# Kernel tuning notes

Measured on AMD Instinct MI355X. Metric: run time of the kernel, lower is better.

## Reference

```python
import jax, jax.numpy as jnp
import numpy as np

TAU = 0.1      # Gumbel-Sinkhorn temperature (module default)
N_ITER = 100   # Sinkhorn iterations (module default)
B, N = 16, 256


def setup_inputs() -> dict:
    key = jax.random.key(0)
    alpha = jax.random.normal(key, (B, N, N), dtype=jnp.float32)
    return {"alpha": alpha}


def _log_sinkhorn(log_alpha, n_iter):
    # Successive row / column normalization in log space.
    # Note: the torch original early-exits once the column sums are within
    # eps=1e-6 of 1; once converged, further iterations are (numerically)
    # identity, so a fixed n_iter loop computes the same result. We use a
    # fixed-length lax.scan, which runs the whole loop on-device with no
    # per-step host sync.
    def step(la, _):
        la = la - jax.nn.logsumexp(la, axis=-1, keepdims=True)  # row normalize
        la = la - jax.nn.logsumexp(la, axis=-2, keepdims=True)  # col normalize
        return la, None

    log_alpha, _ = jax.lax.scan(step, log_alpha, None, length=n_iter)
    return jnp.exp(log_alpha)


def reference(alpha):
    # Training path of GumbelSinkhornPermutation.forward:
    # scale by temperature, then Sinkhorn-normalize to a near doubly-stochastic
    # matrix. (wandb logging side effects omitted.)
    return _log_sinkhorn(alpha / TAU, N_ITER)
```

## Files before the change

kernel.cpp:

```cpp
#include <hip/hip_runtime.h>

#define N_ITER 100

typedef float f32x4 __attribute__((ext_vector_type(4)));
typedef unsigned u32x4 __attribute__((ext_vector_type(4)));

__device__ __forceinline__ unsigned bf16pack(float a, float b) {
  unsigned ua = __float_as_uint(a), ub = __float_as_uint(b);
  ua = (ua + 0x7FFFu + ((ua >> 16) & 1u)) >> 16;
  ub = (ub + 0x7FFFu + ((ub >> 16) & 1u)) >> 16;
  return ua | (ub << 16);
}
__device__ __forceinline__ float bflo(unsigned u) { return __uint_as_float(u << 16); }
__device__ __forceinline__ float bfhi(unsigned u) { return __uint_as_float(u & 0xFFFF0000u); }

__device__ __forceinline__ void pin_agpr(u32x4& x) {
  asm("" : "=a"(x) : "0"(x));
}

__device__ __forceinline__ void mfma_first_nop(f32x4& acc, const u32x4& a, const u32x4& b) {
  asm("s_nop 2\n\tv_mfma_f32_16x16x32_bf16 %0, %1, %2, 0"
      : "=&v"(acc) : "a"(a), "v"(b));
}
__device__ __forceinline__ void mfma_first(f32x4& acc, const u32x4& a, const u32x4& b) {
  asm("v_mfma_f32_16x16x32_bf16 %0, %1, %2, 0"
      : "=&v"(acc) : "a"(a), "v"(b));
}
__device__ __forceinline__ void mfma_aa(f32x4& acc, const u32x4& a, const u32x4& b) {
  asm("v_mfma_f32_16x16x32_bf16 %0, %1, %2, %0"
      : "+v"(acc) : "a"(a), "v"(b));
}
__device__ __forceinline__ void mfma_fence4(f32x4& a0, f32x4& a1, f32x4& a2, f32x4& a3) {
  asm volatile("s_nop 7\n\ts_nop 7\n\ts_nop 7"
               : "+v"(a0), "+v"(a1), "+v"(a2), "+v"(a3));
}

__global__ __launch_bounds__(256)
__attribute__((amdgpu_waves_per_eu(1, 1)))
void sinkhorn_mfma4w(const float* __restrict__ alpha, float* __restrict__ out) {
  __shared__ alignas(16) unsigned short Cb16[256];
  __shared__ alignas(16) unsigned short Rb16[256];
  __shared__ alignas(16) float Cb32[256];
  __shared__ alignas(16) float Rb32[256];

  const int tid  = threadIdx.x;
  const int lane = tid & 63;
  const int w    = tid >> 6;
  const int m    = lane & 15;
  const int q    = lane >> 4;

  const size_t mbase = (size_t)blockIdx.x * (256 * 256);
  const float* A = alpha + mbase;
  float*       O = out + mbase;

  u32x4 arow[4][8];
  u32x4 acol[4][8];

#pragma unroll
  for (int s = 0; s < 4; ++s) {
    const float* rowp = A + (size_t)(64 * w + 16 * s + m) * 256 + 8 * q;
#pragma unroll
    for (int c = 0; c < 8; ++c) {
      float4 x0 = *(const float4*)(rowp + 32 * c);
      float4 x1 = *(const float4*)(rowp + 32 * c + 4);
      arow[s][c] = (u32x4){bf16pack(__expf(x0.x * 10.0f), __expf(x0.y * 10.0f)),
                           bf16pack(__expf(x0.z * 10.0f), __expf(x0.w * 10.0f)),
                           bf16pack(__expf(x1.x * 10.0f), __expf(x1.y * 10.0f)),
                           bf16pack(__expf(x1.z * 10.0f), __expf(x1.w * 10.0f))};
      pin_agpr(arow[s][c]);
    }
    const float* colp = A + (size_t)(8 * q) * 256 + 64 * w + 16 * s + m;
#pragma unroll
    for (int c = 0; c < 8; ++c) {
      const float* p = colp + (size_t)(32 * c) * 256;
      acol[s][c] =
          (u32x4){bf16pack(__expf(p[0] * 10.0f), __expf(p[256] * 10.0f)),
                  bf16pack(__expf(p[512] * 10.0f), __expf(p[768] * 10.0f)),
                  bf16pack(__expf(p[1024] * 10.0f), __expf(p[1280] * 10.0f)),
                  bf16pack(__expf(p[1536] * 10.0f), __expf(p[1792] * 10.0f))};
      pin_agpr(acol[s][c]);
    }
  }

  Cb16[tid] = 0x3F80;
  __syncthreads();

  for (int it = 0; it < N_ITER; ++it) {
    const bool last = (it == N_ITER - 1);

    {
      u32x4 B[8];
#pragma unroll
      for (int c = 0; c < 8; ++c) B[c] = *(const u32x4*)&Cb16[32 * c + 8 * q];
      f32x4 acc0, acc1, acc2, acc3;
      mfma_first_nop(acc0, arow[0][0], B[0]);
      mfma_first(acc1, arow[1][0], B[0]);
      mfma_first(acc2, arow[2][0], B[0]);
      mfma_first(acc3, arow[3][0], B[0]);
#pragma unroll
      for (int c = 1; c < 8; ++c) {
        mfma_aa(acc0, arow[0][c], B[c]);
        mfma_aa(acc1, arow[1][c], B[c]);
        mfma_aa(acc2, arow[2][c], B[c]);
        mfma_aa(acc3, arow[3][c], B[c]);
      }
      mfma_fence4(acc0, acc1, acc2, acc3);
      if (m < 4) {
        f32x4 sA = (m & 1) ? acc1 : acc0;
        f32x4 sB = (m & 1) ? acc3 : acc2;
        f32x4 sv = (m & 2) ? sB : sA;
        float r0 = __builtin_amdgcn_rcpf(sv[0]);
        float r1 = __builtin_amdgcn_rcpf(sv[1]);
        float r2 = __builtin_amdgcn_rcpf(sv[2]);
        float r3 = __builtin_amdgcn_rcpf(sv[3]);
        *(uint2*)&Rb16[64 * w + 16 * m + 4 * q] =
            make_uint2(bf16pack(r0, r1), bf16pack(r2, r3));
        if (last)
          *(float4*)&Rb32[64 * w + 16 * m + 4 * q] = make_float4(r0, r1, r2, r3);
      }
    }
    __syncthreads();

    {
      u32x4 B[8];
#pragma unroll
      for (int c = 0; c < 8; ++c) B[c] = *(const u32x4*)&Rb16[32 * c + 8 * q];
      f32x4 acc0, acc1, acc2, acc3;
      mfma_first_nop(acc0, acol[0][0], B[0]);
      mfma_first(acc1, acol[1][0], B[0]);
      mfma_first(acc2, acol[2][0], B[0]);
      mfma_first(acc3, acol[3][0], B[0]);
#pragma unroll
      for (int c = 1; c < 8; ++c) {
        mfma_aa(acc0, acol[0][c], B[c]);
        mfma_aa(acc1, acol[1][c], B[c]);
        mfma_aa(acc2, acol[2][c], B[c]);
        mfma_aa(acc3, acol[3][c], B[c]);
      }
      mfma_fence4(acc0, acc1, acc2, acc3);
      if (m < 4) {
        f32x4 sA = (m & 1) ? acc1 : acc0;
        f32x4 sB = (m & 1) ? acc3 : acc2;
        f32x4 sv = (m & 2) ? sB : sA;
        float c0 = __builtin_amdgcn_rcpf(sv[0]);
        float c1 = __builtin_amdgcn_rcpf(sv[1]);
        float c2 = __builtin_amdgcn_rcpf(sv[2]);
        float c3 = __builtin_amdgcn_rcpf(sv[3]);
        *(uint2*)&Cb16[64 * w + 16 * m + 4 * q] =
            make_uint2(bf16pack(c0, c1), bf16pack(c2, c3));
        if (last)
          *(float4*)&Cb32[64 * w + 16 * m + 4 * q] = make_float4(c0, c1, c2, c3);
      }
    }
    __syncthreads();
  }

#pragma unroll
  for (int s = 0; s < 4; ++s) {
    const float Rm = Rb32[64 * w + 16 * s + m];
    float* dst = O + (size_t)(64 * w + 16 * s + m) * 256 + 8 * q;
#pragma unroll
    for (int c = 0; c < 8; ++c) {
      float4 c0 = *(const float4*)&Cb32[32 * c + 8 * q];
      float4 c1 = *(const float4*)&Cb32[32 * c + 8 * q + 4];
      u32x4 pk = arow[s][c];
      float4 o0, o1;
      o0.x = bflo(pk.x) * Rm * c0.x;
      o0.y = bfhi(pk.x) * Rm * c0.y;
      o0.z = bflo(pk.y) * Rm * c0.z;
      o0.w = bfhi(pk.y) * Rm * c0.w;
      o1.x = bflo(pk.z) * Rm * c1.x;
      o1.y = bfhi(pk.z) * Rm * c1.y;
      o1.z = bflo(pk.w) * Rm * c1.z;
      o1.w = bfhi(pk.w) * Rm * c1.w;
      *(float4*)(dst + 32 * c) = o0;
      *(float4*)(dst + 32 * c + 4) = o1;
    }
  }
}

extern "C" void kernel_launch(void* const* d_in, const int* in_sizes, int n_in,
                              void* d_out, int out_size, void* d_ws, size_t ws_size,
                              hipStream_t stream) {
  const float* alpha = (const float*)d_in[0];
  float* out = (float*)d_out;
  sinkhorn_mfma4w<<<dim3(16), dim3(256), 0, stream>>>(alpha, out);
}
```

Measured before the change: 174.9 us.

## Split each Sinkhorn matrix across eight waves with independent MFMA accumulator chains

Doubles the block to 512 threads (8 waves, two per SIMD), so each wave holds 2 row-strips and 2 column-strips of the bf16 matrix instead of 4. The k-reduction is split across four independent accumulators per strip, which shortens dependent MFMA chains, and the partial sums are added with vector adds before the reciprocal. This is meant to cut per-iteration MFMA latency in the serial 100-iteration loop. In exchange there are more waves to synchronise at each barrier and extra VALU adds.

```diff
diff --git a/kernel.cpp b/kernel.cpp
--- a/kernel.cpp
+++ b/kernel.cpp
@@ -30,14 +30,16 @@
   asm("v_mfma_f32_16x16x32_bf16 %0, %1, %2, %0"
       : "+v"(acc) : "a"(a), "v"(b));
 }
-__device__ __forceinline__ void mfma_fence4(f32x4& a0, f32x4& a1, f32x4& a2, f32x4& a3) {
+__device__ __forceinline__ void mfma_fence8(f32x4& a0, f32x4& a1, f32x4& a2, f32x4& a3,
+                                            f32x4& a4, f32x4& a5, f32x4& a6, f32x4& a7) {
   asm volatile("s_nop 7\n\ts_nop 7\n\ts_nop 7"
-               : "+v"(a0), "+v"(a1), "+v"(a2), "+v"(a3));
-}
-
-__global__ __launch_bounds__(256)
-__attribute__((amdgpu_waves_per_eu(1, 1)))
-void sinkhorn_mfma4w(const float* __restrict__ alpha, float* __restrict__ out) {
+               : "+v"(a0), "+v"(a1), "+v"(a2), "+v"(a3),
+                 "+v"(a4), "+v"(a5), "+v"(a6), "+v"(a7));
+}
+
+__global__ __launch_bounds__(512)
+__attribute__((amdgpu_waves_per_eu(2, 2)))
+void sinkhorn_mfma8d2(const float* __restrict__ alpha, float* __restrict__ out) {
   __shared__ alignas(16) unsigned short Cb16[256];
   __shared__ alignas(16) unsigned short Rb16[256];
   __shared__ alignas(16) float Cb32[256];
@@ -53,12 +55,12 @@
   const float* A = alpha + mbase;
   float*       O = out + mbase;
 
-  u32x4 arow[4][8];
-  u32x4 acol[4][8];
-
-#pragma unroll
-  for (int s = 0; s < 4; ++s) {
-    const float* rowp = A + (size_t)(64 * w + 16 * s + m) * 256 + 8 * q;
+  u32x4 arow[2][8];
+  u32x4 acol[2][8];
+
+#pragma unroll
+  for (int s = 0; s < 2; ++s) {
+    const float* rowp = A + (size_t)(32 * w + 16 * s + m) * 256 + 8 * q;
 #pragma unroll
     for (int c = 0; c < 8; ++c) {
       float4 x0 = *(const float4*)(rowp + 32 * c);
@@ -67,9 +69,8 @@
                            bf16pack(__expf(x0.z * 10.0f), __expf(x0.w * 10.0f)),
                            bf16pack(__expf(x1.x * 10.0f), __expf(x1.y * 10.0f)),
                            bf16pack(__expf(x1.z * 10.0f), __expf(x1.w * 10.0f))};
-      pin_agpr(arow[s][c]);
-    }
-    const float* colp = A + (size_t)(8 * q) * 256 + 64 * w + 16 * s + m;
+    }
+    const float* colp = A + (size_t)(8 * q) * 256 + 32 * w + 16 * s + m;
 #pragma unroll
     for (int c = 0; c < 8; ++c) {
       const float* p = colp + (size_t)(32 * c) * 256;
@@ -78,11 +79,17 @@
                   bf16pack(__expf(p[512] * 10.0f), __expf(p[768] * 10.0f)),
                   bf16pack(__expf(p[1024] * 10.0f), __expf(p[1280] * 10.0f)),
                   bf16pack(__expf(p[1536] * 10.0f), __expf(p[1792] * 10.0f))};
+    }
+  }
+#pragma unroll
+  for (int s = 0; s < 2; ++s)
+#pragma unroll
+    for (int c = 0; c < 8; ++c) {
+      pin_agpr(arow[s][c]);
       pin_agpr(acol[s][c]);
     }
-  }
-
-  Cb16[tid] = 0x3F80;
+
+  if (tid < 256) Cb16[tid] = 0x3F80;
   __syncthreads();
 
   for (int it = 0; it < N_ITER; ++it) {
@@ -92,31 +99,36 @@
       u32x4 B[8];
 #pragma unroll
       for (int c = 0; c < 8; ++c) B[c] = *(const u32x4*)&Cb16[32 * c + 8 * q];
-      f32x4 acc0, acc1, acc2, acc3;
-      mfma_first_nop(acc0, arow[0][0], B[0]);
-      mfma_first(acc1, arow[1][0], B[0]);
-      mfma_first(acc2, arow[2][0], B[0]);
-      mfma_first(acc3, arow[3][0], B[0]);
-#pragma unroll
-      for (int c = 1; c < 8; ++c) {
-        mfma_aa(acc0, arow[0][c], B[c]);
-        mfma_aa(acc1, arow[1][c], B[c]);
-        mfma_aa(acc2, arow[2][c], B[c]);
-        mfma_aa(acc3, arow[3][c], B[c]);
-      }
-      mfma_fence4(acc0, acc1, acc2, acc3);
-      if (m < 4) {
-        f32x4 sA = (m & 1) ? acc1 : acc0;
-        f32x4 sB = (m & 1) ? acc3 : acc2;
-        f32x4 sv = (m & 2) ? sB : sA;
+      f32x4 a00, a01, a02, a03, a10, a11, a12, a13;
+      mfma_first_nop(a00, arow[0][0], B[0]);
+      mfma_first(a10, arow[1][0], B[0]);
+      mfma_first(a01, arow[0][1], B[1]);
+      mfma_first(a11, arow[1][1], B[1]);
+      mfma_first(a02, arow[0][2], B[2]);
+      mfma_first(a12, arow[1][2], B[2]);
+      mfma_first(a03, arow[0][3], B[3]);
+      mfma_first(a13, arow[1][3], B[3]);
+      mfma_aa(a00, arow[0][4], B[4]);
+      mfma_aa(a10, arow[1][4], B[4]);
+      mfma_aa(a01, arow[0][5], B[5]);
+      mfma_aa(a11, arow[1][5], B[5]);
+      mfma_aa(a02, arow[0][6], B[6]);
+      mfma_aa(a12, arow[1][6], B[6]);
+      mfma_aa(a03, arow[0][7], B[7]);
+      mfma_aa(a13, arow[1][7], B[7]);
+      mfma_fence8(a00, a01, a02, a03, a10, a11, a12, a13);
+      f32x4 s0 = (a00 + a01) + (a02 + a03);
+      f32x4 s1 = (a10 + a11) + (a12 + a13);
+      if (m < 2) {
+        f32x4 sv = m ? s1 : s0;
         float r0 = __builtin_amdgcn_rcpf(sv[0]);
         float r1 = __builtin_amdgcn_rcpf(sv[1]);
         float r2 = __builtin_amdgcn_rcpf(sv[2]);
         float r3 = __builtin_amdgcn_rcpf(sv[3]);
-        *(uint2*)&Rb16[64 * w + 16 * m + 4 * q] =
+        *(uint2*)&Rb16[32 * w + 16 * m + 4 * q] =
             make_uint2(bf16pack(r0, r1), bf16pack(r2, r3));
         if (last)
-          *(float4*)&Rb32[64 * w + 16 * m + 4 * q] = make_float4(r0, r1, r2, r3);
+          *(float4*)&Rb32[32 * w + 16 * m + 4 * q] = make_float4(r0, r1, r2, r3);
       }
     }
     __syncthreads();
@@ -125,40 +137,45 @@
       u32x4 B[8];
 #pragma unroll
       for (int c = 0; c < 8; ++c) B[c] = *(const u32x4*)&Rb16[32 * c + 8 * q];
-      f32x4 acc0, acc1, acc2, acc3;
-      mfma_first_nop(acc0, acol[0][0], B[0]);
-      mfma_first(acc1, acol[1][0], B[0]);
-      mfma_first(acc2, acol[2][0], B[0]);
-      mfma_first(acc3, acol[3][0], B[0]);
-#pragma unroll
-      for (int c = 1; c < 8; ++c) {
-        mfma_aa(acc0, acol[0][c], B[c]);
-        mfma_aa(acc1, acol[1][c], B[c]);
-        mfma_aa(acc2, acol[2][c], B[c]);
-        mfma_aa(acc3, acol[3][c], B[c]);
-      }
-      mfma_fence4(acc0, acc1, acc2, acc3);
-      if (m < 4) {
-        f32x4 sA = (m & 1) ? acc1 : acc0;
-        f32x4 sB = (m & 1) ? acc3 : acc2;
-        f32x4 sv = (m & 2) ? sB : sA;
+      f32x4 a00, a01, a02, a03, a10, a11, a12, a13;
+      mfma_first_nop(a00, acol[0][0], B[0]);
+      mfma_first(a10, acol[1][0], B[0]);
+      mfma_first(a01, acol[0][1], B[1]);
+      mfma_first(a11, acol[1][1], B[1]);
+      mfma_first(a02, acol[0][2], B[2]);
+      mfma_first(a12, acol[1][2], B[2]);
+      mfma_first(a03, acol[0][3], B[3]);
+      mfma_first(a13, acol[1][3], B[3]);
+      mfma_aa(a00, acol[0][4], B[4]);
+      mfma_aa(a10, acol[1][4], B[4]);
+      mfma_aa(a01, acol[0][5], B[5]);
+      mfma_aa(a11, acol[1][5], B[5]);
+      mfma_aa(a02, acol[0][6], B[6]);
+      mfma_aa(a12, acol[1][6], B[6]);
+      mfma_aa(a03, acol[0][7], B[7]);
+      mfma_aa(a13, acol[1][7], B[7]);
+      mfma_fence8(a00, a01, a02, a03, a10, a11, a12, a13);
+      f32x4 s0 = (a00 + a01) + (a02 + a03);
+      f32x4 s1 = (a10 + a11) + (a12 + a13);
+      if (m < 2) {
+        f32x4 sv = m ? s1 : s0;
         float c0 = __builtin_amdgcn_rcpf(sv[0]);
         float c1 = __builtin_amdgcn_rcpf(sv[1]);
         float c2 = __builtin_amdgcn_rcpf(sv[2]);
         float c3 = __builtin_amdgcn_rcpf(sv[3]);
-        *(uint2*)&Cb16[64 * w + 16 * m + 4 * q] =
+        *(uint2*)&Cb16[32 * w + 16 * m + 4 * q] =
             make_uint2(bf16pack(c0, c1), bf16pack(c2, c3));
         if (last)
-          *(float4*)&Cb32[64 * w + 16 * m + 4 * q] = make_float4(c0, c1, c2, c3);
+          *(float4*)&Cb32[32 * w + 16 * m + 4 * q] = make_float4(c0, c1, c2, c3);
       }
     }
     __syncthreads();
   }
 
 #pragma unroll
-  for (int s = 0; s < 4; ++s) {
-    const float Rm = Rb32[64 * w + 16 * s + m];
-    float* dst = O + (size_t)(64 * w + 16 * s + m) * 256 + 8 * q;
+  for (int s = 0; s < 2; ++s) {
+    const float Rm = Rb32[32 * w + 16 * s + m];
+    float* dst = O + (size_t)(32 * w + 16 * s + m) * 256 + 8 * q;
 #pragma unroll
     for (int c = 0; c < 8; ++c) {
       float4 c0 = *(const float4*)&Cb32[32 * c + 8 * q];
@@ -184,5 +201,5 @@
                               hipStream_t stream) {
   const float* alpha = (const float*)d_in[0];
   float* out = (float*)d_out;
-  sinkhorn_mfma4w<<<dim3(16), dim3(256), 0, stream>>>(alpha, out);
-}
+  sinkhorn_mfma8d2<<<dim3(16), dim3(512), 0, stream>>>(alpha, out);
+}
```

After: 186.2 us. 1.06x slower.
